# Kernel optimization log

Hardware: AMD Instinct MI355X
Metric: run time of the kernel (lower is better)

The kernel has to match this reference:

```python
import jax, jax.numpy as jnp
import numpy as np

B, S, D = 2, 2048, 1024
H = 16
HD = D // H  # 64


def setup_inputs() -> dict:
    key = jax.random.key(0)
    k = jax.random.split(key, 6)
    s = 0.02
    return {
        "x": jax.random.normal(k[0], (B, S, D), dtype=jnp.float32),
        "wq": jax.random.normal(k[1], (D, D), dtype=jnp.float32) * s,
        "wk": jax.random.normal(k[2], (D, D), dtype=jnp.float32) * s,
        "wv": jax.random.normal(k[3], (D, D), dtype=jnp.float32) * s,
        "wo": jax.random.normal(k[4], (D, D), dtype=jnp.float32) * s,
        "bo": jnp.zeros((D,), dtype=jnp.float32),
    }


def reference(x, wq, wk, wv, wo, bo):
    b, n, d = x.shape
    # nn.Linear: y = x @ W.T (qkv_bias=False)
    def proj(w):
        y = jnp.einsum('bnd,od->bno', x, w)
        return y.reshape(b, n, H, HD).transpose(0, 2, 1, 3)  # (b, H, n, hd)
    q, k, v = proj(wq), proj(wk), proj(wv)
    scores = jnp.einsum('bhqd,bhkd->bhqk', q, k) / jnp.sqrt(jnp.float32(HD))
    # NOTE: source code slices the causal mask but never applies it; softmax is unmasked.
    attn = jax.nn.softmax(scores, axis=-1)
    # dropout p=0.0 -> identity
    ctx = jnp.einsum('bhqk,bhkd->bhqd', attn, v)
    ctx = ctx.transpose(0, 2, 1, 3).reshape(b, n, d)
    return jnp.einsum('bnd,od->bno', ctx, wo) + bo
```

## Files before the change

### kernel.cpp

```cpp
#include <hip/hip_runtime.h>
#include <hip/hip_bf16.h>
#include <stdint.h>

typedef __attribute__((ext_vector_type(8))) short short8;
typedef __attribute__((ext_vector_type(4))) float float4v;
typedef __attribute__((ext_vector_type(4))) unsigned short ushort4v;

#define Bq 2
#define Sq 2048
#define Dq 1024
#define Hq 16
#define HDq 64

#define QSCALE 0.18033688011112042f

__device__ __forceinline__ unsigned short f2bf(float f) {
  union { float f; uint32_t u; } v; v.f = f;
  uint32_t r = (v.u + 0x7FFFu + ((v.u >> 16) & 1u)) >> 16;
  return (unsigned short)r;
}

__device__ __forceinline__ uint32_t pk2bf(float a, float b) {
  union { __hip_bfloat162 h; uint32_t u; } cv;
  cv.h = __float22bfloat162_rn(make_float2(a, b));
  return cv.u;
}

__device__ __forceinline__ void gl_lds16(const unsigned short* g, unsigned short* l) {
  __builtin_amdgcn_global_load_lds(
      (const __attribute__((address_space(1))) void*)g,
      (__attribute__((address_space(3))) void*)l, 16, 0, 0);
}

__global__ __launch_bounds__(256) void cvt_all_kernel(
    const float* __restrict__ x,
    const float* __restrict__ w0, const float* __restrict__ w1,
    const float* __restrict__ w2, const float* __restrict__ w3,
    unsigned short* __restrict__ xb, unsigned short* __restrict__ wb) {
  const int bid = blockIdx.x;
  const float* src;
  unsigned short* dst;
  int idx;
  if (bid < 4096) {
    src = x; dst = xb;
    idx = bid * 256 + threadIdx.x;
  } else {
    int j = (bid - 4096) * 256 + threadIdx.x;
    int z = j >> 18;
    src = (z == 0) ? w0 : (z == 1) ? w1 : (z == 2) ? w2 : w3;
    dst = wb + (size_t)z * 1048576;
    idx = j & 262143;
  }
  float4v f = ((const float4v*)src)[idx];
  ushort4v o;
#pragma unroll
  for (int q = 0; q < 4; q++) o[q] = f2bf(f[q]);
  ((ushort4v*)dst)[idx] = o;
}

template <bool OUTPROJ, int MT>
__global__ __launch_bounds__(256) void gemm_bt_kernel(
    const unsigned short* __restrict__ A,
    const unsigned short* __restrict__ W0,
    const unsigned short* __restrict__ W1,
    const unsigned short* __restrict__ W2,
    unsigned short* __restrict__ q_dst,
    unsigned short* __restrict__ k_dst,
    unsigned short* __restrict__ v_dst,
    float* __restrict__ f_dst,
    const float* __restrict__ bias) {
  constexpr int K = 1024;
  constexpr int NMB = MT / 32;
  constexpr int APASS = MT / 32;
  const int z = blockIdx.z;
  const unsigned short* W = (z == 0) ? W0 : (z == 1) ? W1 : W2;
  unsigned short* qkv = (z == 0) ? q_dst : (z == 1) ? k_dst : v_dst;

  __shared__ unsigned short Asm[MT * 64];
  __shared__ unsigned short Bsm[128 * 64];

  const int t = threadIdx.x;
  const int wave = t >> 6, lane = t & 63;
  const int quad = lane >> 4, l16 = lane & 15;
  const int wy = wave >> 1, wx = wave & 1;
  const int row0 = blockIdx.x * MT;
  const int col0 = blockIdx.y * 128;

  float4v zero = {0.f, 0.f, 0.f, 0.f};
  float4v acc[NMB][4];
#pragma unroll
  for (int i = 0; i < NMB; i++)
#pragma unroll
    for (int j = 0; j < 4; j++) acc[i][j] = zero;

  const int srow = t >> 3;
  const int sgl = ((t & 7) ^ (srow & 7)) << 3;
  const unsigned short* gA[APASS];
  const unsigned short* gB[4];
#pragma unroll
  for (int i = 0; i < APASS; i++)
    gA[i] = A + (size_t)(row0 + i * 32 + srow) * K + sgl;
#pragma unroll
  for (int i = 0; i < 4; i++)
    gB[i] = W + (size_t)(col0 + i * 32 + srow) * K + sgl;

  const int swl = (l16 & 7);

  for (int k0 = 0; k0 < K; k0 += 64) {
#pragma unroll
    for (int i = 0; i < APASS; i++) gl_lds16(gA[i] + k0, &Asm[i * 2048 + t * 8]);
#pragma unroll
    for (int i = 0; i < 4; i++) gl_lds16(gB[i] + k0, &Bsm[i * 2048 + t * 8]);
    __syncthreads();
    short8 af[NMB][2], bf[4][2];
#pragma unroll
    for (int ks = 0; ks < 2; ks++) {
#pragma unroll
      for (int mb = 0; mb < NMB; mb++) {
        int row = wy * (MT / 2) + mb * 16 + l16;
        int pg = (ks * 4 + quad) ^ swl;
        af[mb][ks] = *(const short8*)(&Asm[row * 64 + pg * 8]);
      }
#pragma unroll
      for (int nb = 0; nb < 4; nb++) {
        int row = wx * 64 + nb * 16 + l16;
        int pg = (ks * 4 + quad) ^ swl;
        bf[nb][ks] = *(const short8*)(&Bsm[row * 64 + pg * 8]);
      }
    }
#pragma unroll
    for (int ks = 0; ks < 2; ks++)
#pragma unroll
      for (int mb = 0; mb < NMB; mb++)
#pragma unroll
        for (int nb = 0; nb < 4; nb++)
          acc[mb][nb] = __builtin_amdgcn_mfma_f32_16x16x32_bf16(af[mb][ks], bf[nb][ks], acc[mb][nb], 0, 0, 0);
    __syncthreads();
  }

  const float qsc = (!OUTPROJ && z == 0) ? QSCALE : 1.0f;
#pragma unroll
  for (int mb = 0; mb < NMB; mb++) {
#pragma unroll
    for (int nb = 0; nb < 4; nb++) {
#pragma unroll
      for (int r = 0; r < 4; r++) {
        int row = row0 + wy * (MT / 2) + mb * 16 + quad * 4 + r;
        int o = col0 + wx * 64 + nb * 16 + l16;
        float val = acc[mb][nb][r];
        if (OUTPROJ) {
          f_dst[(size_t)row * 1024 + o] = val + bias[o];
        } else {
          int b = row >> 11, s = row & 2047;
          int h = o >> 6, hd = o & 63;
          qkv[(size_t)((b * Hq + h) * Sq + s) * HDq + hd] = f2bf(val * qsc);
        }
      }
    }
  }
}

__global__ __launch_bounds__(512, 4) void attn_kernel(
    const unsigned short* __restrict__ Q,
    const unsigned short* __restrict__ Kg,
    const unsigned short* __restrict__ Vg,
    unsigned short* __restrict__ ctx) {
  constexpr int VSTR = 136;
  constexpr int KBUF = 8192;
  constexpr int VBUF = 8704;
  constexpr int QSTR = 132;
  __shared__ __align__(16) unsigned char smem[67584];
  unsigned short* Ksm = (unsigned short*)smem;
  unsigned short* Vsm = (unsigned short*)(smem + 32768);
  float* obuf = (float*)smem;
  float* dbuf = (float*)(smem + 33792);

  const int bh = blockIdx.y;
  const int q0 = blockIdx.x * 128;
  const int t = threadIdx.x;
  const int wave = t >> 6, lane = t & 63;
  const int quad = lane >> 4, l16 = lane & 15;
  const int wq = wave >> 1, wk = wave & 1;
  const int swl = l16 & 7;

  const unsigned short* Qb = Q + (size_t)bh * Sq * HDq;
  const unsigned short* Kb = Kg + (size_t)bh * Sq * HDq;
  const unsigned short* Vb = Vg + (size_t)bh * Sq * HDq;

  short8 qf[2][2];
#pragma unroll
  for (int qb = 0; qb < 2; qb++)
#pragma unroll
    for (int ks = 0; ks < 2; ks++)
      qf[qb][ks] = *(const short8*)(Qb + (size_t)(q0 + wq * 32 + qb * 16 + l16) * HDq + ks * 32 + quad * 8);

  short8 ones;
#pragma unroll
  for (int j = 0; j < 8; j++) ones[j] = (short)0x3F80;

  float4v zero = {0.f, 0.f, 0.f, 0.f};
  float4v of[2][4];
  float4v dsum[2];
#pragma unroll
  for (int qb = 0; qb < 2; qb++) {
    dsum[qb] = zero;
#pragma unroll
    for (int hb = 0; hb < 4; hb++) of[qb][hb] = zero;
  }

  const int srow = t >> 3;
  const unsigned short* gK = Kb + (size_t)srow * 64 + (((t & 7) ^ (srow & 7)) << 3);

  const int vr2 = (t & 63) * 2;
  const int vc8 = (t >> 6) << 3;
  const int sig = (vr2 & ~31) + (((vr2 >> 2) & 3) << 3) + (((vr2 >> 4) & 1) << 2) + (vr2 & 3);
  const unsigned short* gV = Vb + (size_t)vr2 * HDq + vc8;

  short8 vpr0, vpr1;

#define VLOAD(off) do {                                              \
    const unsigned short* vp = gV + (size_t)(off) * HDq;             \
    vpr0 = *(const short8*)(vp);                                     \
    vpr1 = *(const short8*)(vp + HDq);                               \
  } while (0)

#define VPACK(bufsel) do {                                           \
    unsigned short* vd = &Vsm[(bufsel) * VBUF + sig];                \
    _Pragma("unroll")                                                \
    for (int j = 0; j < 8; j++) {                                    \
      uint32_t pk = (uint32_t)(unsigned short)vpr0[j] |              \
                    ((uint32_t)(unsigned short)vpr1[j] << 16);       \
      *(uint32_t*)(vd + (vc8 + j) * VSTR) = pk;                      \
    }                                                                \
  } while (0)

#define KISSUE(off, bufsel) do {                                     \
    gl_lds16(gK + (size_t)(off) * 64, &Ksm[(bufsel) * KBUF + t * 8]);\
    gl_lds16(gK + (size_t)(off) * 64 + 4096,                         \
             &Ksm[(bufsel) * KBUF + 4096 + t * 8]);                  \
  } while (0)

  KISSUE(0, 0);
  VLOAD(0);
  VPACK(0);
  VLOAD(128);
  __syncthreads();
  KISSUE(128, 1);

  for (int kt = 0; kt < Sq; kt += 128) {
    const int cur = (kt >> 7) & 1;
#pragma unroll
    for (int p = 0; p < 2; p++) {
      const int kb0 = cur * KBUF + wk * 4096 + p * 2048;
      short8 kf[2][2];
#pragma unroll
      for (int s = 0; s < 2; s++)
#pragma unroll
        for (int ks = 0; ks < 2; ks++)
          kf[s][ks] = *(const short8*)&Ksm[kb0 + (s * 16 + l16) * 64 + ((ks * 4 + quad) ^ swl) * 8];
      short8 pf[2];
#pragma unroll
      for (int qb = 0; qb < 2; qb++) {
        float4v sa = zero, sb = zero;
#pragma unroll
        for (int ks = 0; ks < 2; ks++) {
          sa = __builtin_amdgcn_mfma_f32_16x16x32_bf16(kf[0][ks], qf[qb][ks], sa, 0, 0, 0);
          sb = __builtin_amdgcn_mfma_f32_16x16x32_bf16(kf[1][ks], qf[qb][ks], sb, 0, 0, 0);
        }
        union { uint32_t u[4]; short8 v; } pw;
        pw.u[0] = pk2bf(__builtin_amdgcn_exp2f(sa[0]), __builtin_amdgcn_exp2f(sa[1]));
        pw.u[1] = pk2bf(__builtin_amdgcn_exp2f(sa[2]), __builtin_amdgcn_exp2f(sa[3]));
        pw.u[2] = pk2bf(__builtin_amdgcn_exp2f(sb[0]), __builtin_amdgcn_exp2f(sb[1]));
        pw.u[3] = pk2bf(__builtin_amdgcn_exp2f(sb[2]), __builtin_amdgcn_exp2f(sb[3]));
        pf[qb] = pw.v;
      }
#pragma unroll
      for (int qb = 0; qb < 2; qb++)
        dsum[qb] = __builtin_amdgcn_mfma_f32_16x16x32_bf16(pf[qb], ones, dsum[qb], 0, 0, 0);
      const int vbo = cur * VBUF + wk * 64 + p * 32 + quad * 8;
#pragma unroll
      for (int hb = 0; hb < 4; hb++) {
        short8 vf = *(const short8*)&Vsm[vbo + (hb * 16 + l16) * VSTR];
#pragma unroll
        for (int qb = 0; qb < 2; qb++)
          of[qb][hb] = __builtin_amdgcn_mfma_f32_16x16x32_bf16(pf[qb], vf, of[qb][hb], 0, 0, 0);
      }
    }
    if (kt + 128 < Sq) VPACK(cur ^ 1);
    if (kt + 256 < Sq) VLOAD(kt + 256);
    __syncthreads();
    if (kt + 256 < Sq) KISSUE(kt + 256, cur);
  }

  if (wk == 0) {
#pragma unroll
    for (int qb = 0; qb < 2; qb++) {
#pragma unroll
      for (int hb = 0; hb < 4; hb++)
        *(float4v*)&obuf[(hb * 16 + l16) * QSTR + wq * 32 + qb * 16 + quad * 4] = of[qb][hb];
      if (l16 == 0)
#pragma unroll
        for (int r = 0; r < 4; r++)
          dbuf[wq * 32 + qb * 16 + quad * 4 + r] = dsum[qb][r];
    }
  }
  __syncthreads();
  if (wk == 1) {
#pragma unroll
    for (int qb = 0; qb < 2; qb++) {
#pragma unroll
      for (int hb = 0; hb < 4; hb++) {
        float4v* pp = (float4v*)&obuf[(hb * 16 + l16) * QSTR + wq * 32 + qb * 16 + quad * 4];
        float4v o = *pp;
        o += of[qb][hb];
        *pp = o;
      }
      if (l16 == 0)
#pragma unroll
        for (int r = 0; r < 4; r++)
          dbuf[wq * 32 + qb * 16 + quad * 4 + r] += dsum[qb][r];
    }
  }
  __syncthreads();

  const int b = bh >> 4, h = bh & 15;
  const int qq = t & 127, hseg = t >> 7;
  const float dinv = 1.0f / dbuf[qq];
  unsigned short* cp = ctx + ((size_t)(b * Sq + q0 + qq)) * Dq + h * 64 + hseg * 16;
  short8 o8a, o8b;
#pragma unroll
  for (int j = 0; j < 8; j++) o8a[j] = (short)f2bf(obuf[(hseg * 16 + j) * QSTR + qq] * dinv);
#pragma unroll
  for (int j = 0; j < 8; j++) o8b[j] = (short)f2bf(obuf[(hseg * 16 + 8 + j) * QSTR + qq] * dinv);
  *(short8*)cp = o8a;
  *(short8*)(cp + 8) = o8b;
#undef VLOAD
#undef VPACK
#undef KISSUE
}

extern "C" void kernel_launch(void* const* d_in, const int* in_sizes, int n_in,
                              void* d_out, int out_size, void* d_ws, size_t ws_size,
                              hipStream_t stream) {
  (void)in_sizes; (void)n_in; (void)out_size; (void)ws_size;
  const float* x  = (const float*)d_in[0];
  const float* wq = (const float*)d_in[1];
  const float* wk = (const float*)d_in[2];
  const float* wv = (const float*)d_in[3];
  const float* wo = (const float*)d_in[4];
  const float* bo = (const float*)d_in[5];
  float* out = (float*)d_out;

  char* ws = (char*)d_ws;
  const size_t MB = 1u << 20;
  unsigned short* xb  = (unsigned short*)(ws + 0 * MB);
  unsigned short* wqb = (unsigned short*)(ws + 8 * MB);
  unsigned short* wkb = (unsigned short*)(ws + 10 * MB);
  unsigned short* wvb = (unsigned short*)(ws + 12 * MB);
  unsigned short* wob = (unsigned short*)(ws + 14 * MB);
  unsigned short* qb  = (unsigned short*)(ws + 16 * MB);
  unsigned short* kb  = (unsigned short*)(ws + 24 * MB);
  unsigned short* vb  = (unsigned short*)(ws + 32 * MB);
  unsigned short* cxb = (unsigned short*)(ws + 40 * MB);

  cvt_all_kernel<<<8192, 256, 0, stream>>>(x, wq, wk, wv, wo, xb, wqb);

  gemm_bt_kernel<false, 128><<<dim3(32, 8, 3), 256, 0, stream>>>(
      xb, wqb, wkb, wvb, qb, kb, vb, nullptr, nullptr);
  attn_kernel<<<dim3(16, 32), 512, 0, stream>>>(qb, kb, vb, cxb);
  gemm_bt_kernel<true, 64><<<dim3(64, 8, 1), 256, 0, stream>>>(
      cxb, wob, wob, wob, nullptr, nullptr, nullptr, out, bo);
}
```

Baseline: 184.2 us.

## Load K tiles into double-buffered registers and swizzle attention grid by XCD

K fragments are now read straight from global memory into two register sets that alternate (ka/kb_), replacing the async global-to-LDS copy and the LDS fragment reads. LDS use drops to only the V buffers, about half the previous allocation, which should allow more workgroups per CU. The grid becomes 1D, and the block index is remapped so that blocks sharing a batch-head land on the same XCD, improving L2 reuse of K and V. In exchange, K global traffic is duplicated across the waves that share key rows, and 64 extra VGPRs under the 512x4 launch bound may cause spills. The final prefetch also reads past the end of each head's K, but those values are never used.

```diff
diff --git a/kernel.cpp b/kernel.cpp
--- a/kernel.cpp
+++ b/kernel.cpp
@@ -166,22 +166,21 @@
     const unsigned short* __restrict__ Vg,
     unsigned short* __restrict__ ctx) {
   constexpr int VSTR = 136;
-  constexpr int KBUF = 8192;
   constexpr int VBUF = 8704;
   constexpr int QSTR = 132;
-  __shared__ __align__(16) unsigned char smem[67584];
-  unsigned short* Ksm = (unsigned short*)smem;
-  unsigned short* Vsm = (unsigned short*)(smem + 32768);
+  __shared__ __align__(16) unsigned char smem[34816];
+  unsigned short* Vsm = (unsigned short*)smem;
   float* obuf = (float*)smem;
   float* dbuf = (float*)(smem + 33792);
 
-  const int bh = blockIdx.y;
-  const int q0 = blockIdx.x * 128;
+  const int wgid = blockIdx.x;
+  const int lid = wgid >> 3;
+  const int bh = (wgid & 7) * 4 + (lid >> 4);
+  const int q0 = (lid & 15) * 128;
   const int t = threadIdx.x;
   const int wave = t >> 6, lane = t & 63;
   const int quad = lane >> 4, l16 = lane & 15;
   const int wq = wave >> 1, wk = wave & 1;
-  const int swl = l16 & 7;
 
   const unsigned short* Qb = Q + (size_t)bh * Sq * HDq;
   const unsigned short* Kb = Kg + (size_t)bh * Sq * HDq;
@@ -208,8 +207,7 @@
     for (int hb = 0; hb < 4; hb++) of[qb][hb] = zero;
   }
 
-  const int srow = t >> 3;
-  const unsigned short* gK = Kb + (size_t)srow * 64 + (((t & 7) ^ (srow & 7)) << 3);
+  const unsigned short* gKf = Kb + (size_t)(wk * 64 + l16) * HDq + quad * 8;
 
   const int vr2 = (t & 63) * 2;
   const int vc8 = (t >> 6) << 3;
@@ -217,6 +215,7 @@
   const unsigned short* gV = Vb + (size_t)vr2 * HDq + vc8;
 
   short8 vpr0, vpr1;
+  short8 ka[8], kb_[8];
 
 #define VLOAD(off) do {                                              \
     const unsigned short* vp = gV + (size_t)(off) * HDq;             \
@@ -234,62 +233,66 @@
     }                                                                \
   } while (0)
 
-#define KISSUE(off, bufsel) do {                                     \
-    gl_lds16(gK + (size_t)(off) * 64, &Ksm[(bufsel) * KBUF + t * 8]);\
-    gl_lds16(gK + (size_t)(off) * 64 + 4096,                         \
-             &Ksm[(bufsel) * KBUF + 4096 + t * 8]);                  \
-  } while (0)
-
-  KISSUE(0, 0);
+#define KLOAD(dst, KT) do {                                          \
+    const unsigned short* kp_ = gKf + (size_t)(KT) * HDq;            \
+    _Pragma("unroll")                                                \
+    for (int p_ = 0; p_ < 2; p_++)                                   \
+      _Pragma("unroll")                                              \
+      for (int s_ = 0; s_ < 2; s_++)                                 \
+        _Pragma("unroll")                                            \
+        for (int ks_ = 0; ks_ < 2; ks_++)                            \
+          dst[p_ * 4 + s_ * 2 + ks_] =                               \
+              *(const short8*)(kp_ + p_ * 2048 + s_ * 1024 + ks_ * 32); \
+  } while (0)
+
+#define PSTEP(kreg, P, BUF) do {                                               \
+    short8 pf[2];                                                              \
+    _Pragma("unroll")                                                          \
+    for (int qb = 0; qb < 2; qb++) {                                           \
+      float4v sa = zero, sb = zero;                                            \
+      _Pragma("unroll")                                                        \
+      for (int ks = 0; ks < 2; ks++) {                                         \
+        sa = __builtin_amdgcn_mfma_f32_16x16x32_bf16(kreg[(P) * 4 + ks], qf[qb][ks], sa, 0, 0, 0);     \
+        sb = __builtin_amdgcn_mfma_f32_16x16x32_bf16(kreg[(P) * 4 + 2 + ks], qf[qb][ks], sb, 0, 0, 0); \
+      }                                                                        \
+      union { uint32_t u[4]; short8 v; } pw;                                   \
+      pw.u[0] = pk2bf(__builtin_amdgcn_exp2f(sa[0]), __builtin_amdgcn_exp2f(sa[1])); \
+      pw.u[1] = pk2bf(__builtin_amdgcn_exp2f(sa[2]), __builtin_amdgcn_exp2f(sa[3])); \
+      pw.u[2] = pk2bf(__builtin_amdgcn_exp2f(sb[0]), __builtin_amdgcn_exp2f(sb[1])); \
+      pw.u[3] = pk2bf(__builtin_amdgcn_exp2f(sb[2]), __builtin_amdgcn_exp2f(sb[3])); \
+      pf[qb] = pw.v;                                                           \
+    }                                                                          \
+    _Pragma("unroll")                                                          \
+    for (int qb = 0; qb < 2; qb++)                                             \
+      dsum[qb] = __builtin_amdgcn_mfma_f32_16x16x32_bf16(pf[qb], ones, dsum[qb], 0, 0, 0); \
+    const int vbo = (BUF) * VBUF + wk * 64 + (P) * 32 + quad * 8;              \
+    _Pragma("unroll")                                                          \
+    for (int hb = 0; hb < 4; hb++) {                                           \
+      short8 vf = *(const short8*)&Vsm[vbo + (hb * 16 + l16) * VSTR];          \
+      _Pragma("unroll")                                                        \
+      for (int qb = 0; qb < 2; qb++)                                           \
+        of[qb][hb] = __builtin_amdgcn_mfma_f32_16x16x32_bf16(pf[qb], vf, of[qb][hb], 0, 0, 0); \
+    }                                                                          \
+  } while (0)
+
+#define TILE(kc, kn, KT, BUF) do {                                   \
+    KLOAD(kn, (KT) + 128);                                           \
+    PSTEP(kc, 0, BUF);                                               \
+    PSTEP(kc, 1, BUF);                                               \
+    if ((KT) + 128 < Sq) VPACK((BUF) ^ 1);                           \
+    if ((KT) + 256 < Sq) VLOAD((KT) + 256);                          \
+    __syncthreads();                                                 \
+  } while (0)
+
+  KLOAD(ka, 0);
   VLOAD(0);
   VPACK(0);
   VLOAD(128);
   __syncthreads();
-  KISSUE(128, 1);
-
-  for (int kt = 0; kt < Sq; kt += 128) {
-    const int cur = (kt >> 7) & 1;
-#pragma unroll
-    for (int p = 0; p < 2; p++) {
-      const int kb0 = cur * KBUF + wk * 4096 + p * 2048;
-      short8 kf[2][2];
-#pragma unroll
-      for (int s = 0; s < 2; s++)
-#pragma unroll
-        for (int ks = 0; ks < 2; ks++)
-          kf[s][ks] = *(const short8*)&Ksm[kb0 + (s * 16 + l16) * 64 + ((ks * 4 + quad) ^ swl) * 8];
-      short8 pf[2];
-#pragma unroll
-      for (int qb = 0; qb < 2; qb++) {
-        float4v sa = zero, sb = zero;
-#pragma unroll
-        for (int ks = 0; ks < 2; ks++) {
-          sa = __builtin_amdgcn_mfma_f32_16x16x32_bf16(kf[0][ks], qf[qb][ks], sa, 0, 0, 0);
-          sb = __builtin_amdgcn_mfma_f32_16x16x32_bf16(kf[1][ks], qf[qb][ks], sb, 0, 0, 0);
-        }
-        union { uint32_t u[4]; short8 v; } pw;
-        pw.u[0] = pk2bf(__builtin_amdgcn_exp2f(sa[0]), __builtin_amdgcn_exp2f(sa[1]));
-        pw.u[1] = pk2bf(__builtin_amdgcn_exp2f(sa[2]), __builtin_amdgcn_exp2f(sa[3]));
-        pw.u[2] = pk2bf(__builtin_amdgcn_exp2f(sb[0]), __builtin_amdgcn_exp2f(sb[1]));
-        pw.u[3] = pk2bf(__builtin_amdgcn_exp2f(sb[2]), __builtin_amdgcn_exp2f(sb[3]));
-        pf[qb] = pw.v;
-      }
-#pragma unroll
-      for (int qb = 0; qb < 2; qb++)
-        dsum[qb] = __builtin_amdgcn_mfma_f32_16x16x32_bf16(pf[qb], ones, dsum[qb], 0, 0, 0);
-      const int vbo = cur * VBUF + wk * 64 + p * 32 + quad * 8;
-#pragma unroll
-      for (int hb = 0; hb < 4; hb++) {
-        short8 vf = *(const short8*)&Vsm[vbo + (hb * 16 + l16) * VSTR];
-#pragma unroll
-        for (int qb = 0; qb < 2; qb++)
-          of[qb][hb] = __builtin_amdgcn_mfma_f32_16x16x32_bf16(pf[qb], vf, of[qb][hb], 0, 0, 0);
-      }
-    }
-    if (kt + 128 < Sq) VPACK(cur ^ 1);
-    if (kt + 256 < Sq) VLOAD(kt + 256);
-    __syncthreads();
-    if (kt + 256 < Sq) KISSUE(kt + 256, cur);
+
+  for (int kt = 0; kt < Sq; kt += 256) {
+    TILE(ka, kb_, kt, 0);
+    TILE(kb_, ka, kt + 128, 1);
   }
 
   if (wk == 0) {
@@ -336,7 +339,9 @@
   *(short8*)(cp + 8) = o8b;
 #undef VLOAD
 #undef VPACK
-#undef KISSUE
+#undef KLOAD
+#undef PSTEP
+#undef TILE
 }
 
 extern "C" void kernel_launch(void* const* d_in, const int* in_sizes, int n_in,
@@ -367,7 +372,7 @@
 
   gemm_bt_kernel<false, 128><<<dim3(32, 8, 3), 256, 0, stream>>>(
       xb, wqb, wkb, wvb, qb, kb, vb, nullptr, nullptr);
-  attn_kernel<<<dim3(16, 32), 512, 0, stream>>>(qb, kb, vb, cxb);
+  attn_kernel<<<dim3(512), 512, 0, stream>>>(qb, kb, vb, cxb);
   gemm_bt_kernel<true, 64><<<dim3(64, 8, 1), 256, 0, stream>>>(
       cxb, wob, wob, wob, nullptr, nullptr, nullptr, out, bo);
 }
```

Measured after the change: 227.8 us. +23.7%, slower.
